# Kernel optimization log

Hardware: AMD Instinct MI355X
Metric: run time of the kernel (lower is better)

The kernel has to match this reference:

```python
import jax, jax.numpy as jnp
import numpy as np

B, N, D, H = 256, 1000, 256, 8
DH = D // H
NEG = -1e9
TANH_CLIP = 10.0


def setup_inputs() -> dict:
    key = jax.random.key(0)
    ks = jax.random.split(key, 16)
    f = jax.random.normal
    return {
        "node_embeddings": f(ks[0], (B, N, D), jnp.float32),
        "graph_context": f(ks[1], (B, D), jnp.float32),
        "glimpse_key": f(ks[2], (B, H, N, DH), jnp.float32),
        "glimpse_val": f(ks[3], (B, H, N, DH), jnp.float32),
        "logit_key": f(ks[4], (B, N, D), jnp.float32),
        "capacity": jax.random.uniform(ks[5], (B, 1, 1), jnp.float32),
        "remaining_demand": jax.random.uniform(ks[6], (B, 1, 1), jnp.float32),
        "remaining_nodes": jax.random.uniform(ks[7], (B, 1, 1), jnp.float32),
        "W_ctx": f(ks[8], (2 * D + 3, 2 * D), jnp.float32) / np.sqrt(2 * D + 3),
        "W_out": f(ks[9], (D, D), jnp.float32) / np.sqrt(D),
        "W_sa": f(ks[10], (D, D), jnp.float32) / np.sqrt(D),
        "head": jax.random.randint(ks[11], (B,), 0, N),
        "feasible_nodes": jax.random.randint(ks[12], (B, N), 0, 2, dtype=jnp.int32),
    }


def _mha(q, k, v, mask):
    # q: [B,H,1,DH]; k,v: [B,H,N,DH]; mask: [B,N] True = feasible
    scores = jnp.einsum('bhqd,bhnd->bhqn', q, k) / np.sqrt(DH)
    scores = jnp.where(mask[:, None, None, :], scores, NEG)
    attn = jax.nn.softmax(scores, axis=-1)
    out = jnp.einsum('bhqn,bhnd->bhqd', attn, v)  # [B,H,1,DH]
    return out.transpose(0, 2, 1, 3).reshape(out.shape[0], D)  # [B,D]


def reference(node_embeddings, graph_context, glimpse_key, glimpse_val,
              logit_key, capacity, remaining_demand, remaining_nodes,
              W_ctx, W_out, W_sa, head, feasible_nodes):
    mask = feasible_nodes.astype(bool)
    no_feasible = ~jnp.any(mask, axis=-1)
    mask = mask.at[:, 0].set(mask[:, 0] | no_feasible)  # force node 0 feasible if all masked

    # dynamic features: [B,3]
    dyn = jnp.concatenate([capacity[:, 0], remaining_demand[:, 0], remaining_nodes[:, 0]], axis=-1)
    # current head node embedding via gather_by_index: [B,D]
    cur = jnp.take_along_axis(node_embeddings, head[:, None, None], axis=1)[:, 0]
    step_context = jnp.concatenate([cur, graph_context, dyn], axis=-1) @ W_ctx  # [B,2D]
    glimpse_q, head_in = step_context[:, :D], step_context[:, D:]

    # glimpse multi-head attention (q_len = 1)
    qh = glimpse_q.reshape(B, 1, H, DH).transpose(0, 2, 1, 3)
    glimpse = _mha(qh, glimpse_key, glimpse_val, mask) @ W_out  # [B,D]

    # single-head pointer logits + tanh clip + masking + log-softmax
    logits = jnp.einsum('bd,bnd->bn', glimpse, logit_key) / np.sqrt(D)
    logits = TANH_CLIP * jnp.tanh(logits)
    logits = jnp.where(mask, logits, NEG)
    log_p = jax.nn.log_softmax(logits, axis=-1)  # [B,N]

    # SimpleSetAttention head encoding over the same cached K/V
    qh2 = head_in.reshape(B, 1, H, DH).transpose(0, 2, 1, 3)
    head_encoding = _mha(qh2, glimpse_key, glimpse_val, mask) @ W_sa  # [B,D]
    return log_p, head_encoding
```

## Files before the change

### kernel.cpp

```cpp
#include <hip/hip_runtime.h>
#include <math.h>

#define B 256
#define N 1000
#define D 256
#define H 8
#define DH 32
#define NEG (-1000000000.0f)

__device__ __forceinline__ float waveReduceMax(float v) {
#pragma unroll
    for (int off = 32; off >= 1; off >>= 1) v = fmaxf(v, __shfl_xor(v, off, 64));
    return v;
}
__device__ __forceinline__ float waveReduceSum(float v) {
#pragma unroll
    for (int off = 32; off >= 1; off >>= 1) v += __shfl_xor(v, off, 64);
    return v;
}
__device__ __forceinline__ float qxor1_add(float v) {
    int t = __builtin_amdgcn_update_dpp(0, __float_as_int(v), 0xB1, 0xF, 0xF, true);
    return v + __int_as_float(t);
}
__device__ __forceinline__ float qxor2_add(float v) {
    int t = __builtin_amdgcn_update_dpp(0, __float_as_int(v), 0x4E, 0xF, 0xF, true);
    return v + __int_as_float(t);
}
__device__ __forceinline__ float sxor4_add(float v) {
    int t = __builtin_amdgcn_ds_swizzle(__float_as_int(v), 0x101F);
    return v + __int_as_float(t);
}
__device__ __forceinline__ float dot4(float4 a, float4 b) {
    return a.x * b.x + a.y * b.y + a.z * b.z + a.w * b.w;
}

__global__ __launch_bounds__(256) void k_ctx(
    const float* __restrict__ ne, const float* __restrict__ gc,
    const float* __restrict__ cap, const float* __restrict__ dem,
    const float* __restrict__ rem, const float* __restrict__ Wctx,
    const int* __restrict__ head,
    float* __restrict__ q1_ws, float* __restrict__ q2_ws)
{
    __shared__ float xs[515];
    const int tid = threadIdx.x;
    const int b = blockIdx.x >> 1;
    const int half = blockIdx.x & 1;
    const int hd = head[b];
    for (int i = tid; i < 515; i += 256) {
        float v;
        if (i < 256)       v = ne[(size_t)(b * N + hd) * D + i];
        else if (i < 512)  v = gc[b * D + (i - 256)];
        else if (i == 512) v = cap[b];
        else if (i == 513) v = dem[b];
        else               v = rem[b];
        xs[i] = v;
    }
    __syncthreads();
    const float* __restrict__ wcol = Wctx + half * 256 + tid;
    float a0 = 0.f, a1 = 0.f, a2 = 0.f, a3 = 0.f;
    int i = 0;
#pragma unroll 2
    for (; i + 4 <= 515; i += 4) {
        a0 = fmaf(xs[i + 0], wcol[(i + 0) * 512], a0);
        a1 = fmaf(xs[i + 1], wcol[(i + 1) * 512], a1);
        a2 = fmaf(xs[i + 2], wcol[(i + 2) * 512], a2);
        a3 = fmaf(xs[i + 3], wcol[(i + 3) * 512], a3);
    }
    for (; i < 515; ++i) a0 = fmaf(xs[i], wcol[i * 512], a0);
    float a = (a0 + a1) + (a2 + a3);
    (half ? q2_ws : q1_ws)[b * D + tid] = a;
}

__global__ __launch_bounds__(1024) void k_mega(
    const float* __restrict__ gk, const float* __restrict__ gv,
    const float* __restrict__ lk,
    const float* __restrict__ q1_ws, const float* __restrict__ q2_ws,
    const float* __restrict__ Wout, const float* __restrict__ Wsa,
    const int* __restrict__ feas,
    float* __restrict__ logp, float* __restrict__ henc_out)
{
    __shared__ float s1[H][N];
    __shared__ float s2[H][N];
    __shared__ int   smask[N];
    __shared__ __align__(16) float q1s[D];
    __shared__ __align__(16) float q2s[D];
    __shared__ int   redOi[16];
    __shared__ float redSum[H][2];
    __shared__ __align__(16) float part1[H][2][DH];
    __shared__ __align__(16) float part2[H][2][DH];
    __shared__ float out1s[D], out2s[D];
    __shared__ float gpart[2][D], hpart[2][D];
    __shared__ __align__(16) float glimpse_s[D];
    __shared__ float logits_s[N];
    __shared__ float redM[16], redS[16];

    const int tid  = threadIdx.x;
    const int b    = blockIdx.x;
    const int wid  = tid >> 6;
    const int lane = tid & 63;

    int mv = (tid < N) ? feas[b * N + tid] : 0;
    int orloc = mv;
#pragma unroll
    for (int off = 32; off >= 1; off >>= 1) orloc |= __shfl_xor(orloc, off, 64);
    if (lane == 0) redOi[wid] = orloc;
    if (tid < 512) {
        float qv = (tid < 256 ? q1_ws : q2_ws)[b * D + (tid & 255)];
        (tid < 256 ? q1s : q2s)[tid & 255] = qv;
    }
    __syncthreads();
    if (tid < N) {
        int anyf = 0;
#pragma unroll
        for (int i = 0; i < 16; ++i) anyf |= redOi[i];
        smask[tid] = (tid == 0 && !anyf) ? 1 : mv;
    }
    __syncthreads();

    const int h    = wid >> 1;
    const int half = wid & 1;
    const int nsub = lane >> 3;
    const int d4   = lane & 7;
    const int r0   = half * 8 + nsub;
    const float4 q1v = ((const float4*)(q1s + h * DH))[d4];
    const float4 q2v = ((const float4*)(q2s + h * DH))[d4];
    const float scale = 0.17677669529663687f;
    const float4* __restrict__ kb = (const float4*)(gk + (size_t)(b * H + h) * N * DH);

#pragma unroll 1
    for (int it = 0; it < 7; ++it) {
        const int rbase = it * 128 + r0;
        float4 kv[8];
#pragma unroll
        for (int k = 0; k < 8; ++k) kv[k] = kb[(rbase + 16 * k) * 8 + d4];
#pragma unroll
        for (int k = 0; k < 8; ++k) {
            float d1 = dot4(kv[k], q1v);
            float d2 = dot4(kv[k], q2v);
            d1 = qxor1_add(d1); d1 = qxor2_add(d1); d1 = sxor4_add(d1);
            d2 = qxor1_add(d2); d2 = qxor2_add(d2); d2 = sxor4_add(d2);
            if (d4 == 0) {
                int r = rbase + 16 * k;
                int m = smask[r];
                s1[h][r] = m ? d1 * scale : NEG;
                s2[h][r] = m ? d2 * scale : NEG;
            }
        }
    }
    {
        float4 kv[8]; int rr[8];
#pragma unroll
        for (int k = 0; k < 8; ++k) {
            rr[k] = 896 + r0 + 16 * k;
            kv[k] = (rr[k] < N) ? kb[rr[k] * 8 + d4] : make_float4(0.f, 0.f, 0.f, 0.f);
        }
#pragma unroll
        for (int k = 0; k < 8; ++k) {
            float d1 = dot4(kv[k], q1v);
            float d2 = dot4(kv[k], q2v);
            d1 = qxor1_add(d1); d1 = qxor2_add(d1); d1 = sxor4_add(d1);
            d2 = qxor1_add(d2); d2 = qxor2_add(d2); d2 = sxor4_add(d2);
            if (d4 == 0 && rr[k] < N) {
                int m = smask[rr[k]];
                s1[h][rr[k]] = m ? d1 * scale : NEG;
                s2[h][rr[k]] = m ? d2 * scale : NEG;
            }
        }
    }
    __syncthreads();

    {
        float* __restrict__ sarr = (wid & 1) ? s2[wid >> 1] : s1[wid >> 1];
        float mx = -INFINITY;
#pragma unroll
        for (int t = 0; t < 16; ++t) {
            int r = lane + 64 * t;
            if (r < N) mx = fmaxf(mx, sarr[r]);
        }
        mx = waveReduceMax(mx);
        float sum = 0.f;
#pragma unroll
        for (int t = 0; t < 16; ++t) {
            int r = lane + 64 * t;
            if (r < N) { float e = __expf(sarr[r] - mx); sarr[r] = e; sum += e; }
        }
        sum = waveReduceSum(sum);
        if (lane == 0) redSum[wid >> 1][wid & 1] = sum;
    }
    __syncthreads();

    const float4* __restrict__ vb = (const float4*)(gv + (size_t)(b * H + h) * N * DH);
    float4 a1 = {0.f, 0.f, 0.f, 0.f}, a2 = {0.f, 0.f, 0.f, 0.f};
#pragma unroll 1
    for (int it = 0; it < 7; ++it) {
        const int rbase = it * 128 + r0;
        float4 vv[8];
#pragma unroll
        for (int k = 0; k < 8; ++k) vv[k] = vb[(rbase + 16 * k) * 8 + d4];
#pragma unroll
        for (int k = 0; k < 8; ++k) {
            int r = rbase + 16 * k;
            float p1 = s1[h][r], p2 = s2[h][r];
            a1.x = fmaf(p1, vv[k].x, a1.x); a1.y = fmaf(p1, vv[k].y, a1.y);
            a1.z = fmaf(p1, vv[k].z, a1.z); a1.w = fmaf(p1, vv[k].w, a1.w);
            a2.x = fmaf(p2, vv[k].x, a2.x); a2.y = fmaf(p2, vv[k].y, a2.y);
            a2.z = fmaf(p2, vv[k].z, a2.z); a2.w = fmaf(p2, vv[k].w, a2.w);
        }
    }
    {
        float4 vv[8]; int rr[8];
#pragma unroll
        for (int k = 0; k < 8; ++k) {
            rr[k] = 896 + r0 + 16 * k;
            vv[k] = (rr[k] < N) ? vb[rr[k] * 8 + d4] : make_float4(0.f, 0.f, 0.f, 0.f);
        }
#pragma unroll
        for (int k = 0; k < 8; ++k) {
            float p1 = (rr[k] < N) ? s1[h][rr[k]] : 0.f;
            float p2 = (rr[k] < N) ? s2[h][rr[k]] : 0.f;
            a1.x = fmaf(p1, vv[k].x, a1.x); a1.y = fmaf(p1, vv[k].y, a1.y);
            a1.z = fmaf(p1, vv[k].z, a1.z); a1.w = fmaf(p1, vv[k].w, a1.w);
            a2.x = fmaf(p2, vv[k].x, a2.x); a2.y = fmaf(p2, vv[k].y, a2.y);
            a2.z = fmaf(p2, vv[k].z, a2.z); a2.w = fmaf(p2, vv[k].w, a2.w);
        }
    }
#pragma unroll
    for (int off = 8; off <= 32; off <<= 1) {
        a1.x += __shfl_xor(a1.x, off, 64); a1.y += __shfl_xor(a1.y, off, 64);
        a1.z += __shfl_xor(a1.z, off, 64); a1.w += __shfl_xor(a1.w, off, 64);
        a2.x += __shfl_xor(a2.x, off, 64); a2.y += __shfl_xor(a2.y, off, 64);
        a2.z += __shfl_xor(a2.z, off, 64); a2.w += __shfl_xor(a2.w, off, 64);
    }
    if (lane < 8) {
        ((float4*)part1[h][half])[d4] = a1;
        ((float4*)part2[h][half])[d4] = a2;
    }
    __syncthreads();
    if (tid < 512) {
        int hh = (tid & 255) >> 5, d = tid & 31;
        if (tid < 256) {
            float rs = 1.f / redSum[hh][0];
            out1s[tid] = (part1[hh][0][d] + part1[hh][1][d]) * rs;
        } else {
            float rs = 1.f / redSum[hh][1];
            out2s[tid - 256] = (part2[hh][0][d] + part2[hh][1][d]) * rs;
        }
    }
    __syncthreads();

    {
        const int col = tid & 255;
        const int seg = (tid >> 8) & 1;
        const bool isG = tid < 512;
        const float* __restrict__ W  = isG ? Wout : Wsa;
        const float* __restrict__ xv = isG ? out1s : out2s;
        const float* __restrict__ Wp = W + (size_t)(seg * 128) * D + col;
        const float* __restrict__ xp = xv + seg * 128;
        float c0 = 0.f, c1 = 0.f, c2 = 0.f, c3 = 0.f;
#pragma unroll 2
        for (int i = 0; i < 128; i += 4) {
            c0 = fmaf(xp[i + 0], Wp[(i + 0) * D], c0);
            c1 = fmaf(xp[i + 1], Wp[(i + 1) * D], c1);
            c2 = fmaf(xp[i + 2], Wp[(i + 2) * D], c2);
            c3 = fmaf(xp[i + 3], Wp[(i + 3) * D], c3);
        }
        (isG ? gpart : hpart)[seg][col] = (c0 + c1) + (c2 + c3);
    }
    __syncthreads();
    if (tid < 256) {
        glimpse_s[tid] = gpart[0][tid] + gpart[1][tid];
    } else if (tid < 512) {
        int c = tid - 256;
        henc_out[b * D + c] = hpart[0][c] + hpart[1][c];
    }
    __syncthreads();

    {
        const int rs = lane >> 3;
        const int c  = lane & 7;
        float4 g[8];
#pragma unroll
        for (int j = 0; j < 8; ++j) g[j] = ((const float4*)glimpse_s)[c + 8 * j];
        const float4* __restrict__ lkb = (const float4*)(lk + (size_t)b * N * D);
#pragma unroll 1
        for (int it = 0; it < 8; ++it) {
            const int r = it * 128 + wid * 8 + rs;
            const bool ok = (r < N);
            float4 kv[8];
#pragma unroll
            for (int j = 0; j < 8; ++j)
                kv[j] = ok ? lkb[(size_t)r * 64 + c + 8 * j]
                           : make_float4(0.f, 0.f, 0.f, 0.f);
            float p = 0.f;
#pragma unroll
            for (int j = 0; j < 8; ++j) p += dot4(kv[j], g[j]);
            p = qxor1_add(p); p = qxor2_add(p); p = sxor4_add(p);
            if (c == 0 && ok) {
                float l = 10.0f * tanhf(p * 0.0625f);
                logits_s[r] = smask[r] ? l : NEG;
            }
        }
    }
    __syncthreads();

    {
        float v = (tid < N) ? logits_s[tid] : -INFINITY;
        float m = waveReduceMax(v);
        if (lane == 0) redM[wid] = m;
        __syncthreads();
        m = redM[0];
#pragma unroll
        for (int i = 1; i < 16; ++i) m = fmaxf(m, redM[i]);
        float e = (tid < N) ? __expf(v - m) : 0.f;
        float s = waveReduceSum(e);
        if (lane == 0) redS[wid] = s;
        __syncthreads();
        s = 0.f;
#pragma unroll
        for (int i = 0; i < 16; ++i) s += redS[i];
        const float lse = m + logf(s);
        if (tid < N) logp[b * N + tid] = v - lse;
    }
}

extern "C" void kernel_launch(void* const* d_in, const int* in_sizes, int n_in,
                              void* d_out, int out_size, void* d_ws, size_t ws_size,
                              hipStream_t stream) {
    const float* ne   = (const float*)d_in[0];
    const float* gc   = (const float*)d_in[1];
    const float* gk   = (const float*)d_in[2];
    const float* gvv  = (const float*)d_in[3];
    const float* lk   = (const float*)d_in[4];
    const float* cap  = (const float*)d_in[5];
    const float* dem  = (const float*)d_in[6];
    const float* rem  = (const float*)d_in[7];
    const float* Wctx = (const float*)d_in[8];
    const float* Wout = (const float*)d_in[9];
    const float* Wsa  = (const float*)d_in[10];
    const int*   head = (const int*)d_in[11];
    const int*   feas = (const int*)d_in[12];
    float* out = (float*)d_out;

    float* ws    = (float*)d_ws;
    float* q1_ws = ws;
    float* q2_ws = q1_ws + B * D;

    hipLaunchKernelGGL(k_ctx, dim3(B * 2), dim3(256), 0, stream,
                       ne, gc, cap, dem, rem, Wctx, head, q1_ws, q2_ws);
    hipLaunchKernelGGL(k_mega, dim3(B), dim3(1024), 0, stream,
                       gk, gvv, lk, q1_ws, q2_ws, Wout, Wsa, feas,
                       out, out + B * N);
}
```

Measured before the change: 791.5 us.

## Split mega kernel into per-head flash-attention blocks plus separate tail kernel

The attention part of the per-batch 1024-thread mega kernel moves into a new kernel with one 256-thread block per (batch, head). It uses an online-softmax (flash-style) single pass that loads K and V together, so the shared score arrays and the second pass over scores go away. Mask preprocessing moves to its own small kernel, and the projection/logit tail runs in a separate kernel that reads attention outputs from workspace. This gives 2048 smaller blocks instead of 256 large ones, which should improve occupancy and memory-level parallelism, at the cost of two extra launches and workspace round trips.

```diff
diff --git a/kernel.cpp b/kernel.cpp
--- a/kernel.cpp
+++ b/kernel.cpp
@@ -32,6 +32,37 @@
 }
 __device__ __forceinline__ float dot4(float4 a, float4 b) {
     return a.x * b.x + a.y * b.y + a.z * b.z + a.w * b.w;
+}
+
+__global__ __launch_bounds__(256) void k_mask(
+    const int* __restrict__ feas, int* __restrict__ mask_ws)
+{
+    __shared__ int sRed[4];
+    const int b = blockIdx.x;
+    const int tid = threadIdx.x;
+    int vals[4];
+    int orloc = 0;
+#pragma unroll
+    for (int k = 0; k < 4; ++k) {
+        int n = tid + k * 256;
+        int v = (n < N) ? feas[b * N + n] : 0;
+        vals[k] = v;
+        orloc |= v;
+    }
+#pragma unroll
+    for (int off = 32; off >= 1; off >>= 1) orloc |= __shfl_xor(orloc, off, 64);
+    if ((tid & 63) == 0) sRed[tid >> 6] = orloc;
+    __syncthreads();
+    const int anyf = sRed[0] | sRed[1] | sRed[2] | sRed[3];
+#pragma unroll
+    for (int k = 0; k < 4; ++k) {
+        int n = tid + k * 256;
+        if (n < N) {
+            int m = vals[k];
+            if (n == 0 && !anyf) m = 1;
+            mask_ws[b * N + n] = m;
+        }
+    }
 }
 
 __global__ __launch_bounds__(256) void k_ctx(
@@ -71,23 +102,185 @@
     (half ? q2_ws : q1_ws)[b * D + tid] = a;
 }
 
-__global__ __launch_bounds__(1024) void k_mega(
+__global__ __launch_bounds__(256) void k_fattn(
     const float* __restrict__ gk, const float* __restrict__ gv,
+    const float* __restrict__ q1_ws, const float* __restrict__ q2_ws,
+    const int* __restrict__ mask_ws,
+    float* __restrict__ out1_ws, float* __restrict__ out2_ws)
+{
+    __shared__ int smask[N];
+    __shared__ float mrg[4][8][12];
+
+    const int tid  = threadIdx.x;
+    const int b    = blockIdx.x >> 3;
+    const int h    = blockIdx.x & 7;
+    const int wid  = tid >> 6;
+    const int lane = tid & 63;
+    const int nsub = lane >> 3;
+    const int d4   = lane & 7;
+
+    for (int i = tid; i < N; i += 256) smask[i] = mask_ws[b * N + i];
+
+    const float4 q1v = ((const float4*)(q1_ws + (size_t)b * D + h * DH))[d4];
+    const float4 q2v = ((const float4*)(q2_ws + (size_t)b * D + h * DH))[d4];
+    const float scale = 0.17677669529663687f;
+    const float4* __restrict__ kb = (const float4*)(gk + (size_t)(b * H + h) * N * DH);
+    const float4* __restrict__ vb = (const float4*)(gv + (size_t)(b * H + h) * N * DH);
+    const int r0 = wid * 8 + nsub;
+    __syncthreads();
+
+    float m1 = -1e30f, m2 = -1e30f, sum1 = 0.f, sum2 = 0.f;
+    float4 a1 = {0.f, 0.f, 0.f, 0.f}, a2 = {0.f, 0.f, 0.f, 0.f};
+
+#pragma unroll 1
+    for (int it = 0; it < 3; ++it) {
+        const int rb = it * 256 + r0;
+        float4 kv[8], vv[8];
+#pragma unroll
+        for (int k = 0; k < 8; ++k) kv[k] = kb[(rb + 32 * k) * 8 + d4];
+#pragma unroll
+        for (int k = 0; k < 8; ++k) vv[k] = vb[(rb + 32 * k) * 8 + d4];
+
+        float s1v[8], s2v[8];
+#pragma unroll
+        for (int k = 0; k < 8; ++k) {
+            float d1 = dot4(kv[k], q1v);
+            float d2 = dot4(kv[k], q2v);
+            d1 = qxor1_add(d1); d1 = qxor2_add(d1); d1 = sxor4_add(d1);
+            d2 = qxor1_add(d2); d2 = qxor2_add(d2); d2 = sxor4_add(d2);
+            int mm = smask[rb + 32 * k];
+            s1v[k] = mm ? d1 * scale : NEG;
+            s2v[k] = mm ? d2 * scale : NEG;
+        }
+        float tm1 = s1v[0], tm2 = s2v[0];
+#pragma unroll
+        for (int k = 1; k < 8; ++k) { tm1 = fmaxf(tm1, s1v[k]); tm2 = fmaxf(tm2, s2v[k]); }
+        float M1 = fmaxf(m1, tm1), M2 = fmaxf(m2, tm2);
+        float f1 = __expf(m1 - M1), f2 = __expf(m2 - M2);
+        sum1 *= f1; sum2 *= f2;
+        a1.x *= f1; a1.y *= f1; a1.z *= f1; a1.w *= f1;
+        a2.x *= f2; a2.y *= f2; a2.z *= f2; a2.w *= f2;
+        m1 = M1; m2 = M2;
+#pragma unroll
+        for (int k = 0; k < 8; ++k) {
+            float e1 = __expf(s1v[k] - m1);
+            float e2 = __expf(s2v[k] - m2);
+            sum1 += e1; sum2 += e2;
+            a1.x = fmaf(e1, vv[k].x, a1.x); a1.y = fmaf(e1, vv[k].y, a1.y);
+            a1.z = fmaf(e1, vv[k].z, a1.z); a1.w = fmaf(e1, vv[k].w, a1.w);
+            a2.x = fmaf(e2, vv[k].x, a2.x); a2.y = fmaf(e2, vv[k].y, a2.y);
+            a2.z = fmaf(e2, vv[k].z, a2.z); a2.w = fmaf(e2, vv[k].w, a2.w);
+        }
+    }
+    {
+        float4 kv[8], vv[8]; int rr[8];
+#pragma unroll
+        for (int k = 0; k < 8; ++k) {
+            rr[k] = 768 + r0 + 32 * k;
+            kv[k] = (rr[k] < N) ? kb[rr[k] * 8 + d4] : make_float4(0.f, 0.f, 0.f, 0.f);
+        }
+#pragma unroll
+        for (int k = 0; k < 8; ++k)
+            vv[k] = (rr[k] < N) ? vb[rr[k] * 8 + d4] : make_float4(0.f, 0.f, 0.f, 0.f);
+
+        float s1v[8], s2v[8];
+#pragma unroll
+        for (int k = 0; k < 8; ++k) {
+            float d1 = dot4(kv[k], q1v);
+            float d2 = dot4(kv[k], q2v);
+            d1 = qxor1_add(d1); d1 = qxor2_add(d1); d1 = sxor4_add(d1);
+            d2 = qxor1_add(d2); d2 = qxor2_add(d2); d2 = sxor4_add(d2);
+            int mm = (rr[k] < N) ? smask[rr[k]] : 0;
+            s1v[k] = mm ? d1 * scale : NEG;
+            s2v[k] = mm ? d2 * scale : NEG;
+        }
+        float tm1 = s1v[0], tm2 = s2v[0];
+#pragma unroll
+        for (int k = 1; k < 8; ++k) { tm1 = fmaxf(tm1, s1v[k]); tm2 = fmaxf(tm2, s2v[k]); }
+        float M1 = fmaxf(m1, tm1), M2 = fmaxf(m2, tm2);
+        float f1 = __expf(m1 - M1), f2 = __expf(m2 - M2);
+        sum1 *= f1; sum2 *= f2;
+        a1.x *= f1; a1.y *= f1; a1.z *= f1; a1.w *= f1;
+        a2.x *= f2; a2.y *= f2; a2.z *= f2; a2.w *= f2;
+        m1 = M1; m2 = M2;
+#pragma unroll
+        for (int k = 0; k < 8; ++k) {
+            float e1 = __expf(s1v[k] - m1);
+            float e2 = __expf(s2v[k] - m2);
+            sum1 += e1; sum2 += e2;
+            a1.x = fmaf(e1, vv[k].x, a1.x); a1.y = fmaf(e1, vv[k].y, a1.y);
+            a1.z = fmaf(e1, vv[k].z, a1.z); a1.w = fmaf(e1, vv[k].w, a1.w);
+            a2.x = fmaf(e2, vv[k].x, a2.x); a2.y = fmaf(e2, vv[k].y, a2.y);
+            a2.z = fmaf(e2, vv[k].z, a2.z); a2.w = fmaf(e2, vv[k].w, a2.w);
+        }
+    }
+
+#pragma unroll
+    for (int off = 8; off <= 32; off <<= 1) {
+        float om1 = __shfl_xor(m1, off, 64), os1 = __shfl_xor(sum1, off, 64);
+        float4 oa1;
+        oa1.x = __shfl_xor(a1.x, off, 64); oa1.y = __shfl_xor(a1.y, off, 64);
+        oa1.z = __shfl_xor(a1.z, off, 64); oa1.w = __shfl_xor(a1.w, off, 64);
+        float M = fmaxf(m1, om1);
+        float g1 = __expf(m1 - M), g2 = __expf(om1 - M);
+        sum1 = sum1 * g1 + os1 * g2;
+        a1.x = a1.x * g1 + oa1.x * g2; a1.y = a1.y * g1 + oa1.y * g2;
+        a1.z = a1.z * g1 + oa1.z * g2; a1.w = a1.w * g1 + oa1.w * g2;
+        m1 = M;
+
+        float om2 = __shfl_xor(m2, off, 64), os2 = __shfl_xor(sum2, off, 64);
+        float4 oa2;
+        oa2.x = __shfl_xor(a2.x, off, 64); oa2.y = __shfl_xor(a2.y, off, 64);
+        oa2.z = __shfl_xor(a2.z, off, 64); oa2.w = __shfl_xor(a2.w, off, 64);
+        float M2m = fmaxf(m2, om2);
+        float h1 = __expf(m2 - M2m), h2 = __expf(om2 - M2m);
+        sum2 = sum2 * h1 + os2 * h2;
+        a2.x = a2.x * h1 + oa2.x * h2; a2.y = a2.y * h1 + oa2.y * h2;
+        a2.z = a2.z * h1 + oa2.z * h2; a2.w = a2.w * h1 + oa2.w * h2;
+        m2 = M2m;
+    }
+
+    if (lane < 8) {
+        float* p = mrg[wid][d4];
+        p[0] = m1; p[1] = sum1; p[2] = a1.x; p[3] = a1.y; p[4] = a1.z; p[5] = a1.w;
+        p[6] = m2; p[7] = sum2; p[8] = a2.x; p[9] = a2.y; p[10] = a2.z; p[11] = a2.w;
+    }
+    __syncthreads();
+    if (tid < 8) {
+        float M1 = -1e30f, S1 = 0.f; float4 A1 = {0.f, 0.f, 0.f, 0.f};
+        float M2 = -1e30f, S2 = 0.f; float4 A2 = {0.f, 0.f, 0.f, 0.f};
+#pragma unroll
+        for (int w = 0; w < 4; ++w) {
+            const float* p = mrg[w][tid];
+            float nm = fmaxf(M1, p[0]);
+            float ga = __expf(M1 - nm), gb = __expf(p[0] - nm);
+            S1 = S1 * ga + p[1] * gb;
+            A1.x = A1.x * ga + p[2] * gb; A1.y = A1.y * ga + p[3] * gb;
+            A1.z = A1.z * ga + p[4] * gb; A1.w = A1.w * ga + p[5] * gb;
+            M1 = nm;
+            nm = fmaxf(M2, p[6]);
+            ga = __expf(M2 - nm); gb = __expf(p[6] - nm);
+            S2 = S2 * ga + p[7] * gb;
+            A2.x = A2.x * ga + p[8] * gb; A2.y = A2.y * ga + p[9] * gb;
+            A2.z = A2.z * ga + p[10] * gb; A2.w = A2.w * ga + p[11] * gb;
+            M2 = nm;
+        }
+        float r1 = 1.f / S1, r2 = 1.f / S2;
+        float4 o1 = { A1.x * r1, A1.y * r1, A1.z * r1, A1.w * r1 };
+        float4 o2 = { A2.x * r2, A2.y * r2, A2.z * r2, A2.w * r2 };
+        ((float4*)(out1_ws + (size_t)b * D + h * DH))[tid] = o1;
+        ((float4*)(out2_ws + (size_t)b * D + h * DH))[tid] = o2;
+    }
+}
+
+__global__ __launch_bounds__(1024) void k_tail(
+    const float* __restrict__ out1_ws, const float* __restrict__ out2_ws,
     const float* __restrict__ lk,
-    const float* __restrict__ q1_ws, const float* __restrict__ q2_ws,
     const float* __restrict__ Wout, const float* __restrict__ Wsa,
-    const int* __restrict__ feas,
+    const int* __restrict__ mask_ws,
     float* __restrict__ logp, float* __restrict__ henc_out)
 {
-    __shared__ float s1[H][N];
-    __shared__ float s2[H][N];
-    __shared__ int   smask[N];
-    __shared__ __align__(16) float q1s[D];
-    __shared__ __align__(16) float q2s[D];
-    __shared__ int   redOi[16];
-    __shared__ float redSum[H][2];
-    __shared__ __align__(16) float part1[H][2][DH];
-    __shared__ __align__(16) float part2[H][2][DH];
+    __shared__ int smask[N];
     __shared__ float out1s[D], out2s[D];
     __shared__ float gpart[2][D], hpart[2][D];
     __shared__ __align__(16) float glimpse_s[D];
@@ -99,153 +292,11 @@
     const int wid  = tid >> 6;
     const int lane = tid & 63;
 
-    int mv = (tid < N) ? feas[b * N + tid] : 0;
-    int orloc = mv;
-#pragma unroll
-    for (int off = 32; off >= 1; off >>= 1) orloc |= __shfl_xor(orloc, off, 64);
-    if (lane == 0) redOi[wid] = orloc;
     if (tid < 512) {
-        float qv = (tid < 256 ? q1_ws : q2_ws)[b * D + (tid & 255)];
-        (tid < 256 ? q1s : q2s)[tid & 255] = qv;
-    }
-    __syncthreads();
-    if (tid < N) {
-        int anyf = 0;
-#pragma unroll
-        for (int i = 0; i < 16; ++i) anyf |= redOi[i];
-        smask[tid] = (tid == 0 && !anyf) ? 1 : mv;
-    }
-    __syncthreads();
-
-    const int h    = wid >> 1;
-    const int half = wid & 1;
-    const int nsub = lane >> 3;
-    const int d4   = lane & 7;
-    const int r0   = half * 8 + nsub;
-    const float4 q1v = ((const float4*)(q1s + h * DH))[d4];
-    const float4 q2v = ((const float4*)(q2s + h * DH))[d4];
-    const float scale = 0.17677669529663687f;
-    const float4* __restrict__ kb = (const float4*)(gk + (size_t)(b * H + h) * N * DH);
-
-#pragma unroll 1
-    for (int it = 0; it < 7; ++it) {
-        const int rbase = it * 128 + r0;
-        float4 kv[8];
-#pragma unroll
-        for (int k = 0; k < 8; ++k) kv[k] = kb[(rbase + 16 * k) * 8 + d4];
-#pragma unroll
-        for (int k = 0; k < 8; ++k) {
-            float d1 = dot4(kv[k], q1v);
-            float d2 = dot4(kv[k], q2v);
-            d1 = qxor1_add(d1); d1 = qxor2_add(d1); d1 = sxor4_add(d1);
-            d2 = qxor1_add(d2); d2 = qxor2_add(d2); d2 = sxor4_add(d2);
-            if (d4 == 0) {
-                int r = rbase + 16 * k;
-                int m = smask[r];
-                s1[h][r] = m ? d1 * scale : NEG;
-                s2[h][r] = m ? d2 * scale : NEG;
-            }
-        }
-    }
-    {
-        float4 kv[8]; int rr[8];
-#pragma unroll
-        for (int k = 0; k < 8; ++k) {
-            rr[k] = 896 + r0 + 16 * k;
-            kv[k] = (rr[k] < N) ? kb[rr[k] * 8 + d4] : make_float4(0.f, 0.f, 0.f, 0.f);
-        }
-#pragma unroll
-        for (int k = 0; k < 8; ++k) {
-            float d1 = dot4(kv[k], q1v);
-            float d2 = dot4(kv[k], q2v);
-            d1 = qxor1_add(d1); d1 = qxor2_add(d1); d1 = sxor4_add(d1);
-            d2 = qxor1_add(d2); d2 = qxor2_add(d2); d2 = sxor4_add(d2);
-            if (d4 == 0 && rr[k] < N) {
-                int m = smask[rr[k]];
-                s1[h][rr[k]] = m ? d1 * scale : NEG;
-                s2[h][rr[k]] = m ? d2 * scale : NEG;
-            }
-        }
-    }
-    __syncthreads();
-
-    {
-        float* __restrict__ sarr = (wid & 1) ? s2[wid >> 1] : s1[wid >> 1];
-        float mx = -INFINITY;
-#pragma unroll
-        for (int t = 0; t < 16; ++t) {
-            int r = lane + 64 * t;
-            if (r < N) mx = fmaxf(mx, sarr[r]);
-        }
-        mx = waveReduceMax(mx);
-        float sum = 0.f;
-#pragma unroll
-        for (int t = 0; t < 16; ++t) {
-            int r = lane + 64 * t;
-            if (r < N) { float e = __expf(sarr[r] - mx); sarr[r] = e; sum += e; }
-        }
-        sum = waveReduceSum(sum);
-        if (lane == 0) redSum[wid >> 1][wid & 1] = sum;
-    }
-    __syncthreads();
-
-    const float4* __restrict__ vb = (const float4*)(gv + (size_t)(b * H + h) * N * DH);
-    float4 a1 = {0.f, 0.f, 0.f, 0.f}, a2 = {0.f, 0.f, 0.f, 0.f};
-#pragma unroll 1
-    for (int it = 0; it < 7; ++it) {
-        const int rbase = it * 128 + r0;
-        float4 vv[8];
-#pragma unroll
-        for (int k = 0; k < 8; ++k) vv[k] = vb[(rbase + 16 * k) * 8 + d4];
-#pragma unroll
-        for (int k = 0; k < 8; ++k) {
-            int r = rbase + 16 * k;
-            float p1 = s1[h][r], p2 = s2[h][r];
-            a1.x = fmaf(p1, vv[k].x, a1.x); a1.y = fmaf(p1, vv[k].y, a1.y);
-            a1.z = fmaf(p1, vv[k].z, a1.z); a1.w = fmaf(p1, vv[k].w, a1.w);
-            a2.x = fmaf(p2, vv[k].x, a2.x); a2.y = fmaf(p2, vv[k].y, a2.y);
-            a2.z = fmaf(p2, vv[k].z, a2.z); a2.w = fmaf(p2, vv[k].w, a2.w);
-        }
-    }
-    {
-        float4 vv[8]; int rr[8];
-#pragma unroll
-        for (int k = 0; k < 8; ++k) {
-            rr[k] = 896 + r0 + 16 * k;
-            vv[k] = (rr[k] < N) ? vb[rr[k] * 8 + d4] : make_float4(0.f, 0.f, 0.f, 0.f);
-        }
-#pragma unroll
-        for (int k = 0; k < 8; ++k) {
-            float p1 = (rr[k] < N) ? s1[h][rr[k]] : 0.f;
-            float p2 = (rr[k] < N) ? s2[h][rr[k]] : 0.f;
-            a1.x = fmaf(p1, vv[k].x, a1.x); a1.y = fmaf(p1, vv[k].y, a1.y);
-            a1.z = fmaf(p1, vv[k].z, a1.z); a1.w = fmaf(p1, vv[k].w, a1.w);
-            a2.x = fmaf(p2, vv[k].x, a2.x); a2.y = fmaf(p2, vv[k].y, a2.y);
-            a2.z = fmaf(p2, vv[k].z, a2.z); a2.w = fmaf(p2, vv[k].w, a2.w);
-        }
-    }
-#pragma unroll
-    for (int off = 8; off <= 32; off <<= 1) {
-        a1.x += __shfl_xor(a1.x, off, 64); a1.y += __shfl_xor(a1.y, off, 64);
-        a1.z += __shfl_xor(a1.z, off, 64); a1.w += __shfl_xor(a1.w, off, 64);
-        a2.x += __shfl_xor(a2.x, off, 64); a2.y += __shfl_xor(a2.y, off, 64);
-        a2.z += __shfl_xor(a2.z, off, 64); a2.w += __shfl_xor(a2.w, off, 64);
-    }
-    if (lane < 8) {
-        ((float4*)part1[h][half])[d4] = a1;
-        ((float4*)part2[h][half])[d4] = a2;
-    }
-    __syncthreads();
-    if (tid < 512) {
-        int hh = (tid & 255) >> 5, d = tid & 31;
-        if (tid < 256) {
-            float rs = 1.f / redSum[hh][0];
-            out1s[tid] = (part1[hh][0][d] + part1[hh][1][d]) * rs;
-        } else {
-            float rs = 1.f / redSum[hh][1];
-            out2s[tid - 256] = (part2[hh][0][d] + part2[hh][1][d]) * rs;
-        }
-    }
+        float v = (tid < 256 ? out1_ws : out2_ws)[b * D + (tid & 255)];
+        (tid < 256 ? out1s : out2s)[tid & 255] = v;
+    }
+    if (tid < N) smask[tid] = mask_ws[b * N + tid];
     __syncthreads();
 
     {
@@ -341,13 +392,19 @@
     const int*   feas = (const int*)d_in[12];
     float* out = (float*)d_out;
 
-    float* ws    = (float*)d_ws;
-    float* q1_ws = ws;
-    float* q2_ws = q1_ws + B * D;
-
+    float* ws      = (float*)d_ws;
+    float* q1_ws   = ws;
+    float* q2_ws   = q1_ws + B * D;
+    int*   mask_ws = (int*)(q2_ws + B * D);
+    float* out1_ws = (float*)(mask_ws + B * N);
+    float* out2_ws = out1_ws + B * D;
+
+    hipLaunchKernelGGL(k_mask, dim3(B), dim3(256), 0, stream, feas, mask_ws);
     hipLaunchKernelGGL(k_ctx, dim3(B * 2), dim3(256), 0, stream,
                        ne, gc, cap, dem, rem, Wctx, head, q1_ws, q2_ws);
-    hipLaunchKernelGGL(k_mega, dim3(B), dim3(1024), 0, stream,
-                       gk, gvv, lk, q1_ws, q2_ws, Wout, Wsa, feas,
+    hipLaunchKernelGGL(k_fattn, dim3(B * H), dim3(256), 0, stream,
+                       gk, gvv, q1_ws, q2_ws, mask_ws, out1_ws, out2_ws);
+    hipLaunchKernelGGL(k_tail, dim3(B), dim3(1024), 0, stream,
+                       out1_ws, out2_ws, lk, Wout, Wsa, mask_ws,
                        out, out + B * N);
 }
```

Result: no change. 805.6 us (+1.8%).
